# Kernel tuning notes

Measured on AMD Instinct MI355X. Metric: run time of the kernel, lower is better.

## Reference

```python
import jax, jax.numpy as jnp
import numpy as np

IN_DIMS = 1024
K = 8


def setup_inputs() -> dict:
    key = jax.random.key(0)
    ks = jax.random.split(key, 7)
    s = 1.0 / np.sqrt(IN_DIMS)
    x = jax.random.normal(ks[0], (8, 2048, IN_DIMS), dtype=jnp.float32)
    Wq = jax.random.uniform(ks[1], (IN_DIMS, K), jnp.float32, -s, s)
    bq = jax.random.uniform(ks[2], (K,), jnp.float32, -s, s)
    Wk = jax.random.uniform(ks[3], (IN_DIMS, K), jnp.float32, -s, s)
    bk = jax.random.uniform(ks[4], (K,), jnp.float32, -s, s)
    Wv = jax.random.uniform(ks[5], (IN_DIMS, IN_DIMS), jnp.float32, -s, s)
    bv = jax.random.uniform(ks[6], (IN_DIMS,), jnp.float32, -s, s)
    return {"x": x, "Wq": Wq, "bq": bq, "Wk": Wk, "bk": bk, "Wv": Wv, "bv": bv}


def reference(x, Wq, bq, Wk, bk, Wv, bv):
    # x: [B,S,D]; rank-k projections
    q = jnp.einsum('bsd,dk->bsk', x, Wq) + bq        # [B,S,k]
    k = jnp.einsum('bsd,dk->bsk', x, Wk) + bk        # [B,S,k]
    energy = jnp.einsum('bik,bjk->bij', q, k)        # [B,S,S] (unscaled)
    attention = jax.nn.softmax(energy, axis=-1)
    value = jnp.einsum('bsd,de->bse', x, Wv) + bv    # [B,S,D]
    out = jnp.einsum('bij,bjd->bid', attention, value)
    return (out, attention)
```

## Files before the change

kernel.cpp:

```cpp
#include <hip/hip_runtime.h>


typedef __attribute__((ext_vector_type(8))) __bf16 bf16x8;
typedef __attribute__((ext_vector_type(4))) __bf16 bf16x4;
typedef __attribute__((ext_vector_type(4))) float  f32x4;
typedef unsigned int u32;

#define GLB_CAST(p) ((const __attribute__((address_space(1))) u32*)(p))
#define LDS_CAST(p) ((__attribute__((address_space(3))) u32*)(p))

#define S_BARRIER() { __builtin_amdgcn_s_barrier(); __builtin_amdgcn_sched_barrier(0); }
#define LGKM0()     { asm volatile("s_waitcnt lgkmcnt(0)" ::: "memory"); __builtin_amdgcn_sched_barrier(0); }
#define VMCNT8()    { asm volatile("s_waitcnt vmcnt(8)" ::: "memory"); __builtin_amdgcn_sched_barrier(0); }
#define VMCNT0()    { asm volatile("s_waitcnt vmcnt(0)" ::: "memory"); __builtin_amdgcn_sched_barrier(0); }

static constexpr int    Bn   = 8;
static constexpr int    S    = 2048;
static constexpr int    Dd   = 1024;
static constexpr int    Mtot = Bn * S;
static constexpr size_t OUT0 = (size_t)Bn * S * Dd;

static constexpr size_t OFF_XBF  = 0;
static constexpr size_t OFF_WVT  = OFF_XBF  + (size_t)Mtot * Dd * 2;
static constexpr size_t OFF_WQKT = OFF_WVT  + (size_t)Dd * Dd * 2;
static constexpr size_t OFF_Q    = OFF_WQKT + (size_t)16 * Dd * 2;
static constexpr size_t OFF_K    = OFF_Q    + (size_t)Mtot * 8 * 4;
static constexpr size_t OFF_VT   = OFF_K    + (size_t)Mtot * 8 * 4;
static constexpr size_t OFF_ATTB = OFF_VT   + (size_t)Bn * Dd * S * 2;
static constexpr size_t WS_NEED  = OFF_ATTB + (size_t)Bn * S * S * 2;

__global__ __launch_bounds__(256) void prep_kernel(
    const float* __restrict__ x, const float* __restrict__ Wq,
    const float* __restrict__ Wk, const float* __restrict__ Wv,
    __bf16* __restrict__ xbf, __bf16* __restrict__ wvt, __bf16* __restrict__ wqkT)
{
    __shared__ float lt[64][65];
    int bid = blockIdx.x, t = threadIdx.x;
    if (bid < 4096) {
        #pragma unroll
        for (int i = 0; i < 4; ++i) {
            size_t idx4 = (size_t)i * 1048576 + (size_t)bid * 256 + t;
            f32x4 v = ((const f32x4*)x)[idx4];
            bf16x4 o;
            #pragma unroll
            for (int c = 0; c < 4; ++c) o[c] = (__bf16)v[c];
            ((bf16x4*)xbf)[idx4] = o;
        }
    } else if (bid < 4352) {
        int tile = bid - 4096;
        int tr = tile >> 4, tc = tile & 15;
        int r0 = t >> 6, c = t & 63;
        #pragma unroll
        for (int i = 0; i < 16; ++i) {
            int row = i * 4 + r0;
            lt[row][c] = Wv[(size_t)(tr * 64 + row) * 1024 + tc * 64 + c];
        }
        __syncthreads();
        #pragma unroll
        for (int i = 0; i < 16; ++i) {
            int er = i * 4 + r0;
            wvt[(size_t)(tc * 64 + er) * 1024 + tr * 64 + c] = (__bf16)lt[c][er];
        }
    } else {
        int lb = bid - 4352;
        #pragma unroll
        for (int i = 0; i < 4; ++i) {
            int idx = (lb * 4 + i) * 256 + t;
            int n = idx >> 10, d = idx & 1023;
            float v = (n < 8) ? Wq[d * 8 + n] : Wk[d * 8 + (n & 7)];
            wqkT[n * 1024 + d] = (__bf16)v;
        }
    }
}

__global__ __launch_bounds__(256) void qk_proj_kernel(
    const __bf16* __restrict__ xbf, const __bf16* __restrict__ wqkT,
    const float* __restrict__ bq, const float* __restrict__ bk,
    float* __restrict__ qb, float* __restrict__ kb)
{
    int t = threadIdx.x, l = t & 63, w = t >> 6;
    int mbase = (blockIdx.x * 4 + w) * 16;
    f32x4 acc = {0.f, 0.f, 0.f, 0.f};
    const __bf16* ar = xbf + (size_t)(mbase + (l & 15)) * 1024 + ((l >> 4) << 3);
    const __bf16* br = wqkT + (size_t)(l & 15) * 1024 + ((l >> 4) << 3);
    #pragma unroll 8
    for (int kk = 0; kk < 1024; kk += 32) {
        bf16x8 a = *(const bf16x8*)(ar + kk);
        bf16x8 b = *(const bf16x8*)(br + kk);
        acc = __builtin_amdgcn_mfma_f32_16x16x32_bf16(a, b, acc, 0, 0, 0);
    }
    int n = l & 15;
    float bias = (n < 8) ? bq[n] : bk[n & 7];
    #pragma unroll
    for (int r = 0; r < 4; ++r) {
        int m = mbase + ((l >> 4) << 2) + r;
        float v = acc[r] + bias;
        if (n < 8) qb[m * 8 + n] = v;
        else       kb[m * 8 + (n & 7)] = v;
    }
}

__global__ __launch_bounds__(256) void softmax_kernel(
    const float* __restrict__ qb, const float* __restrict__ kb,
    float* __restrict__ attnF, __bf16* __restrict__ attnB)
{
    int bid = blockIdx.x;
    int b = bid >> 6, chunk = bid & 63;
    int t = threadIdx.x, l = t & 63, w = t >> 6;
    float kr[8][8];
    const float* kbb = kb + ((size_t)b << 14);
    #pragma unroll
    for (int jj = 0; jj < 8; ++jj) {
        f32x4 v0 = *(const f32x4*)(kbb + (size_t)(t * 8 + jj) * 8);
        f32x4 v1 = *(const f32x4*)(kbb + (size_t)(t * 8 + jj) * 8 + 4);
        #pragma unroll
        for (int c = 0; c < 4; ++c) { kr[jj][c] = v0[c]; kr[jj][4 + c] = v1[c]; }
    }
    __shared__ float redm[4], reds[4];
    const float* qrow = qb + ((size_t)b << 14);
    for (int ii = 0; ii < 32; ++ii) {
        int i = (chunk << 5) + ii;
        f32x4 q0 = *(const f32x4*)(qrow + (size_t)i * 8);
        f32x4 q1 = *(const f32x4*)(qrow + (size_t)i * 8 + 4);
        float e[8];
        #pragma unroll
        for (int jj = 0; jj < 8; ++jj) {
            float s = q0[0] * kr[jj][0];
            s = fmaf(q0[1], kr[jj][1], s);
            s = fmaf(q0[2], kr[jj][2], s);
            s = fmaf(q0[3], kr[jj][3], s);
            s = fmaf(q1[0], kr[jj][4], s);
            s = fmaf(q1[1], kr[jj][5], s);
            s = fmaf(q1[2], kr[jj][6], s);
            s = fmaf(q1[3], kr[jj][7], s);
            e[jj] = s;
        }
        float mx = e[0];
        #pragma unroll
        for (int jj = 1; jj < 8; ++jj) mx = fmaxf(mx, e[jj]);
        #pragma unroll
        for (int d = 1; d < 64; d <<= 1) mx = fmaxf(mx, __shfl_xor(mx, d));
        if (l == 0) redm[w] = mx;
        __syncthreads();
        mx = fmaxf(fmaxf(redm[0], redm[1]), fmaxf(redm[2], redm[3]));
        float p[8], sum = 0.f;
        #pragma unroll
        for (int jj = 0; jj < 8; ++jj) { p[jj] = __expf(e[jj] - mx); sum += p[jj]; }
        #pragma unroll
        for (int d = 1; d < 64; d <<= 1) sum += __shfl_xor(sum, d);
        if (l == 0) reds[w] = sum;
        __syncthreads();
        float T = (reds[0] + reds[1]) + (reds[2] + reds[3]);
        float inv = 1.0f / T;
        size_t off = (((size_t)b << 11) + i) * 2048 + (size_t)t * 8;
        f32x4 o0, o1; bf16x8 ob;
        #pragma unroll
        for (int c = 0; c < 4; ++c) {
            o0[c] = p[c] * inv; o1[c] = p[4 + c] * inv;
            ob[c] = (__bf16)o0[c]; ob[4 + c] = (__bf16)o1[c];
        }
        *(f32x4*)(attnF + off) = o0;
        *(f32x4*)(attnF + off + 4) = o1;
        *(bf16x8*)(attnB + off) = ob;
    }
}

template<int LDA>
__device__ __forceinline__ void stageA(const __bf16* Ab, char* smem,
    int slot, int kk, int c, int rowin, int sl8, int wid)
{
    __builtin_amdgcn_global_load_lds(
        GLB_CAST(Ab + (size_t)(c * 64 + rowin) * LDA + kk + sl8 * 8),
        LDS_CAST(smem + slot * 65536 + c * 8192 + wid * 1024), 16, 0, 0);
}
template<int LDA>
__device__ __forceinline__ void stageB(const __bf16* Bb, char* smem,
    int slot, int kk, int c, int rowin, int sl8, int wid)
{
    __builtin_amdgcn_global_load_lds(
        GLB_CAST(Bb + (size_t)(c * 64 + rowin) * LDA + kk + sl8 * 8),
        LDS_CAST(smem + slot * 65536 + 32768 + c * 8192 + wid * 1024), 16, 0, 0);
}

template<int MODE>
__global__ __launch_bounds__(512, 2) void gemm_kernel(
    const __bf16* __restrict__ A, const __bf16* __restrict__ Bt,
    float* __restrict__ outF, __bf16* __restrict__ outVt,
    const float* __restrict__ bv)
{
    constexpr int LDA = (MODE == 0) ? 1024 : 2048;
    constexpr int NT  = LDA / 64;
    __shared__ __align__(1024) char smem[131072];

    int bid = blockIdx.x;
    int wg = ((bid & 7) << 5) | (bid >> 3);
    int t = threadIdx.x, l = t & 63;
    int wid = t >> 6;
    int wmr = wid >> 2, wnc = wid & 3;

    int mblk, nblk, bb = 0;
    size_t aoff, boff;
    if constexpr (MODE == 0) {
        mblk = wg >> 2; nblk = wg & 3;
        aoff = (size_t)mblk * 256 * LDA; boff = 0;
    } else {
        bb = wg >> 5; int r = wg & 31;
        mblk = r >> 2; nblk = r & 3;
        aoff = (size_t)bb * S * S + (size_t)mblk * 256 * LDA;
        boff = (size_t)bb * Dd * S;
    }
    const __bf16* Ab = A + aoff;
    const __bf16* Bb = Bt + boff + (size_t)nblk * 256 * LDA;

    int rowin = t >> 3;
    int sl8 = (t & 7) ^ (rowin & 7);
    int lr = l & 15, lk = l >> 4;

    f32x4 acc[8][4] = {};

    #pragma unroll
    for (int c = 0; c < 4; ++c) {
        stageA<LDA>(Ab, smem, 0, 0, c, rowin, sl8, wid);
        stageB<LDA>(Bb, smem, 0, 0, c, rowin, sl8, wid);
    }
    #pragma unroll
    for (int c = 0; c < 4; ++c) {
        stageA<LDA>(Ab, smem, 1, 64, c, rowin, sl8, wid);
        stageB<LDA>(Bb, smem, 1, 64, c, rowin, sl8, wid);
    }
    VMCNT8();
    S_BARRIER();

    for (int tt = 0; tt < NT; ++tt) {
        int s = tt & 1;
        const __bf16* Asl = (const __bf16*)(smem + s * 65536);
        const __bf16* Bsl = (const __bf16*)(smem + s * 65536 + 32768);
        bool pf = (tt + 2 < NT);
        int kk2 = (tt + 2) * 64;

        bf16x8 aLo[2][4], aHi[2][4], bLo[2][2], bHi[2][2];

        #pragma unroll
        for (int ks = 0; ks < 2; ++ks) {
            int sa = ks * 4 + lk;
            #pragma unroll
            for (int i = 0; i < 4; ++i) {
                int ra = wmr * 128 + i * 16 + lr;
                aLo[ks][i] = *(const bf16x8*)&Asl[ra * 64 + ((sa ^ (ra & 7)) << 3)];
            }
            #pragma unroll
            for (int j = 0; j < 2; ++j) {
                int rb = wnc * 64 + j * 16 + lr;
                bLo[ks][j] = *(const bf16x8*)&Bsl[rb * 64 + ((sa ^ (rb & 7)) << 3)];
            }
        }
        S_BARRIER(); LGKM0();
        __builtin_amdgcn_s_setprio(1);
        #pragma unroll
        for (int ks = 0; ks < 2; ++ks)
            #pragma unroll
            for (int i = 0; i < 4; ++i)
                #pragma unroll
                for (int j = 0; j < 2; ++j)
                    acc[i][j] = __builtin_amdgcn_mfma_f32_16x16x32_bf16(aLo[ks][i], bLo[ks][j], acc[i][j], 0, 0, 0);
        __builtin_amdgcn_s_setprio(0);
        S_BARRIER();

        #pragma unroll
        for (int ks = 0; ks < 2; ++ks) {
            int sa = ks * 4 + lk;
            #pragma unroll
            for (int j = 0; j < 2; ++j) {
                int rb = wnc * 64 + (j + 2) * 16 + lr;
                bHi[ks][j] = *(const bf16x8*)&Bsl[rb * 64 + ((sa ^ (rb & 7)) << 3)];
            }
        }
        if (pf) {
            stageA<LDA>(Ab, smem, s, kk2, 0, rowin, sl8, wid);
            stageA<LDA>(Ab, smem, s, kk2, 2, rowin, sl8, wid);
        }
        S_BARRIER(); LGKM0();
        __builtin_amdgcn_s_setprio(1);
        #pragma unroll
        for (int ks = 0; ks < 2; ++ks)
            #pragma unroll
            for (int i = 0; i < 4; ++i)
                #pragma unroll
                for (int j = 0; j < 2; ++j)
                    acc[i][2 + j] = __builtin_amdgcn_mfma_f32_16x16x32_bf16(aLo[ks][i], bHi[ks][j], acc[i][2 + j], 0, 0, 0);
        __builtin_amdgcn_s_setprio(0);
        S_BARRIER();

        #pragma unroll
        for (int ks = 0; ks < 2; ++ks) {
            int sa = ks * 4 + lk;
            #pragma unroll
            for (int i = 0; i < 4; ++i) {
                int ra = wmr * 128 + (i + 4) * 16 + lr;
                aHi[ks][i] = *(const bf16x8*)&Asl[ra * 64 + ((sa ^ (ra & 7)) << 3)];
            }
        }
        if (pf) {
            #pragma unroll
            for (int c = 0; c < 4; ++c)
                stageB<LDA>(Bb, smem, s, kk2, c, rowin, sl8, wid);
        }
        S_BARRIER(); LGKM0();
        __builtin_amdgcn_s_setprio(1);
        #pragma unroll
        for (int ks = 0; ks < 2; ++ks)
            #pragma unroll
            for (int i = 0; i < 4; ++i)
                #pragma unroll
                for (int j = 0; j < 2; ++j)
                    acc[4 + i][2 + j] = __builtin_amdgcn_mfma_f32_16x16x32_bf16(aHi[ks][i], bHi[ks][j], acc[4 + i][2 + j], 0, 0, 0);
        __builtin_amdgcn_s_setprio(0);
        S_BARRIER();

        if (pf) {
            stageA<LDA>(Ab, smem, s, kk2, 1, rowin, sl8, wid);
            stageA<LDA>(Ab, smem, s, kk2, 3, rowin, sl8, wid);
        }
        S_BARRIER();
        __builtin_amdgcn_s_setprio(1);
        #pragma unroll
        for (int ks = 0; ks < 2; ++ks)
            #pragma unroll
            for (int i = 0; i < 4; ++i)
                #pragma unroll
                for (int j = 0; j < 2; ++j)
                    acc[4 + i][j] = __builtin_amdgcn_mfma_f32_16x16x32_bf16(aHi[ks][i], bLo[ks][j], acc[4 + i][j], 0, 0, 0);
        __builtin_amdgcn_s_setprio(0);

        if (tt == NT - 1) break;
        S_BARRIER();
        if (pf) { VMCNT8(); } else { VMCNT0(); }
        S_BARRIER();
    }

    if constexpr (MODE == 0) {
        #pragma unroll
        for (int j = 0; j < 4; ++j) {
            int e = (nblk << 8) + wnc * 64 + j * 16 + lr;
            float bias = bv[e];
            #pragma unroll
            for (int i = 0; i < 8; ++i) {
                int m0 = (mblk << 8) + wmr * 128 + i * 16 + (lk << 2);
                int b = m0 >> 11, s0 = m0 & 2047;
                bf16x4 o;
                #pragma unroll
                for (int r = 0; r < 4; ++r) o[r] = (__bf16)(acc[i][j][r] + bias);
                *(bf16x4*)&outVt[(((size_t)(b << 10) + e) << 11) + s0] = o;
            }
        }
    } else {
        float* ob = outF + (size_t)bb * S * Dd;
        #pragma unroll
        for (int i = 0; i < 8; ++i) {
            int m0 = (mblk << 8) + wmr * 128 + i * 16 + (lk << 2);
            #pragma unroll
            for (int j = 0; j < 4; ++j) {
                int e = (nblk << 8) + wnc * 64 + j * 16 + lr;
                #pragma unroll
                for (int r = 0; r < 4; ++r)
                    ob[(size_t)(m0 + r) * 1024 + e] = acc[i][j][r];
            }
        }
    }
}

extern "C" void kernel_launch(void* const* d_in, const int* in_sizes, int n_in,
                              void* d_out, int out_size, void* d_ws, size_t ws_size,
                              hipStream_t stream)
{
    const float* x  = (const float*)d_in[0];
    const float* Wq = (const float*)d_in[1];
    const float* bq = (const float*)d_in[2];
    const float* Wk = (const float*)d_in[3];
    const float* bk = (const float*)d_in[4];
    const float* Wv = (const float*)d_in[5];
    const float* bv = (const float*)d_in[6];

    float* outp  = (float*)d_out;
    float* attnF = outp + OUT0;

    if (ws_size < WS_NEED) return;
    char* ws = (char*)d_ws;
    __bf16* xbf   = (__bf16*)(ws + OFF_XBF);
    __bf16* wvt   = (__bf16*)(ws + OFF_WVT);
    __bf16* wqkT  = (__bf16*)(ws + OFF_WQKT);
    float*  qbuf  = (float*)(ws + OFF_Q);
    float*  kbuf  = (float*)(ws + OFF_K);
    __bf16* vt    = (__bf16*)(ws + OFF_VT);
    __bf16* attnB = (__bf16*)(ws + OFF_ATTB);

    prep_kernel<<<4368, 256, 0, stream>>>(x, Wq, Wk, Wv, xbf, wvt, wqkT);
    qk_proj_kernel<<<256, 256, 0, stream>>>(xbf, wqkT, bq, bk, qbuf, kbuf);
    gemm_kernel<0><<<256, 512, 0, stream>>>(xbf, wvt, nullptr, vt, bv);
    softmax_kernel<<<512, 256, 0, stream>>>(qbuf, kbuf, attnF, attnB);
    gemm_kernel<1><<<256, 512, 0, stream>>>(attnB, vt, outp, nullptr, nullptr);
}
```

Baseline: 196.3 us.

## Fuse value-projection GEMM and softmax into one interleaved heterogeneous launch

Merges the x·Wv GEMM and the softmax kernel into a single launch whose blocks are interleaved by segment: some blocks run a new, smaller 128x128-tile single-buffered GEMM and others run the softmax. The aim is to overlap the compute-bound GEMM with the store-bound softmax (which writes the large fp32 and bf16 attention matrices) and to remove one kernel boundary. In exchange, the value GEMM loses the highly tuned 256x256 double-buffered pipeline. It now uses a simpler kernel with a sync per K-step, which may make the GEMM itself slower.

Measured after the change: 187.1 us. 4.7% less time.

```diff
diff --git a/kernel.cpp b/kernel.cpp
--- a/kernel.cpp
+++ b/kernel.cpp
@@ -21,12 +21,12 @@
 static constexpr size_t OUT0 = (size_t)Bn * S * Dd;
 
 static constexpr size_t OFF_XBF  = 0;
-static constexpr size_t OFF_WVT  = OFF_XBF  + (size_t)Mtot * Dd * 2;
-static constexpr size_t OFF_WQKT = OFF_WVT  + (size_t)Dd * Dd * 2;
+static constexpr size_t OFF_WVT  = OFF_XBF + (size_t)Mtot * Dd * 2;
+static constexpr size_t OFF_WQKT = OFF_WVT + (size_t)Dd * Dd * 2;
 static constexpr size_t OFF_Q    = OFF_WQKT + (size_t)16 * Dd * 2;
-static constexpr size_t OFF_K    = OFF_Q    + (size_t)Mtot * 8 * 4;
-static constexpr size_t OFF_VT   = OFF_K    + (size_t)Mtot * 8 * 4;
-static constexpr size_t OFF_ATTB = OFF_VT   + (size_t)Bn * Dd * S * 2;
+static constexpr size_t OFF_K    = OFF_Q   + (size_t)Mtot * 8 * 4;
+static constexpr size_t OFF_VT   = OFF_K   + (size_t)Mtot * 8 * 4;
+static constexpr size_t OFF_ATTB = OFF_VT  + (size_t)Bn * Dd * S * 2;
 static constexpr size_t WS_NEED  = OFF_ATTB + (size_t)Bn * S * S * 2;
 
 __global__ __launch_bounds__(256) void prep_kernel(
@@ -100,96 +100,176 @@
     }
 }
 
-__global__ __launch_bounds__(256) void softmax_kernel(
+__global__ __launch_bounds__(256) void fused_gs_kernel(
+    const __bf16* __restrict__ xbf, const __bf16* __restrict__ wvt,
+    const float* __restrict__ bv,
     const float* __restrict__ qb, const float* __restrict__ kb,
-    float* __restrict__ attnF, __bf16* __restrict__ attnB)
-{
-    int bid = blockIdx.x;
-    int b = bid >> 6, chunk = bid & 63;
-    int t = threadIdx.x, l = t & 63, w = t >> 6;
-    float kr[8][8];
-    const float* kbb = kb + ((size_t)b << 14);
-    #pragma unroll
-    for (int jj = 0; jj < 8; ++jj) {
-        f32x4 v0 = *(const f32x4*)(kbb + (size_t)(t * 8 + jj) * 8);
-        f32x4 v1 = *(const f32x4*)(kbb + (size_t)(t * 8 + jj) * 8 + 4);
-        #pragma unroll
-        for (int c = 0; c < 4; ++c) { kr[jj][c] = v0[c]; kr[jj][4 + c] = v1[c]; }
-    }
+    __bf16* __restrict__ vtOut, float* __restrict__ attnF,
+    __bf16* __restrict__ attnB)
+{
+    __shared__ __align__(1024) char smem[32768];
     __shared__ float redm[4], reds[4];
-    const float* qrow = qb + ((size_t)b << 14);
-    for (int ii = 0; ii < 32; ++ii) {
-        int i = (chunk << 5) + ii;
-        f32x4 q0 = *(const f32x4*)(qrow + (size_t)i * 8);
-        f32x4 q1 = *(const f32x4*)(qrow + (size_t)i * 8 + 4);
-        float e[8];
+    int bid = blockIdx.x, t = threadIdx.x;
+    int seg = bid >> 8;
+    int gid = -1, sid = -1;
+    if (seg == 0) gid = bid;
+    else if (seg == 1) sid = bid - 256;
+    else if (seg == 2) gid = bid - 256;
+    else if (seg == 3) sid = bid - 512;
+    else gid = bid - 512;
+
+    if (sid < 0) {
+        int g = ((gid & 7) << 7) | (gid >> 3);
+        int mblk = g >> 3, nblk = g & 7;
+        int l = t & 63, wid = t >> 6;
+        int wmr = wid >> 1, wnc = wid & 1;
+        int lr = l & 15, lk = l >> 4;
+
+        int srow = t >> 3;
+        int ssl  = (t & 7) ^ (srow & 7);
+        const __bf16* gA = xbf + (size_t)(mblk * 128 + srow) * 1024 + ssl * 8;
+        const __bf16* gB = wvt + (size_t)(nblk * 128 + srow) * 1024 + ssl * 8;
+
+        int s0 = (lk ^ (lr & 7)) << 3;
+        int s1 = ((lk ^ 4) ^ (lr & 7)) << 3;
+        int offA0 = (wmr * 64 + lr) * 64 + s0;
+        int offA1 = (wmr * 64 + lr) * 64 + s1;
+        int offB0 = (wnc * 64 + lr) * 64 + s0;
+        int offB1 = (wnc * 64 + lr) * 64 + s1;
+
+        f32x4 acc[4][4] = {};
+
+        for (int tt = 0; tt < 16; ++tt) {
+            int kk = tt * 64;
+            #pragma unroll
+            for (int c = 0; c < 4; ++c) {
+                __builtin_amdgcn_global_load_lds(
+                    GLB_CAST(gA + (size_t)c * 32 * 1024 + kk),
+                    LDS_CAST(smem + c * 4096 + wid * 1024), 16, 0, 0);
+                __builtin_amdgcn_global_load_lds(
+                    GLB_CAST(gB + (size_t)c * 32 * 1024 + kk),
+                    LDS_CAST(smem + 16384 + c * 4096 + wid * 1024), 16, 0, 0);
+            }
+            __syncthreads();
+            const __bf16* As = (const __bf16*)smem;
+            const __bf16* Bs = (const __bf16*)(smem + 16384);
+            bf16x8 af[4], bfr[4];
+            #pragma unroll
+            for (int i = 0; i < 4; ++i) af[i]  = *(const bf16x8*)(As + offA0 + i * 1024);
+            #pragma unroll
+            for (int j = 0; j < 4; ++j) bfr[j] = *(const bf16x8*)(Bs + offB0 + j * 1024);
+            #pragma unroll
+            for (int i = 0; i < 4; ++i)
+                #pragma unroll
+                for (int j = 0; j < 4; ++j)
+                    acc[i][j] = __builtin_amdgcn_mfma_f32_16x16x32_bf16(af[i], bfr[j], acc[i][j], 0, 0, 0);
+            #pragma unroll
+            for (int i = 0; i < 4; ++i) af[i]  = *(const bf16x8*)(As + offA1 + i * 1024);
+            #pragma unroll
+            for (int j = 0; j < 4; ++j) bfr[j] = *(const bf16x8*)(Bs + offB1 + j * 1024);
+            #pragma unroll
+            for (int i = 0; i < 4; ++i)
+                #pragma unroll
+                for (int j = 0; j < 4; ++j)
+                    acc[i][j] = __builtin_amdgcn_mfma_f32_16x16x32_bf16(af[i], bfr[j], acc[i][j], 0, 0, 0);
+            __syncthreads();
+        }
+
+        #pragma unroll
+        for (int j = 0; j < 4; ++j) {
+            int e = (nblk << 7) + wnc * 64 + j * 16 + lr;
+            float bias = bv[e];
+            #pragma unroll
+            for (int i = 0; i < 4; ++i) {
+                int m0 = (mblk << 7) + wmr * 64 + i * 16 + (lk << 2);
+                int b = m0 >> 11, sA = m0 & 2047;
+                bf16x4 o;
+                #pragma unroll
+                for (int r = 0; r < 4; ++r) o[r] = (__bf16)(acc[i][j][r] + bias);
+                *(bf16x4*)&vtOut[(((size_t)(b << 10) + e) << 11) + sA] = o;
+            }
+        }
+    } else {
+        int b = sid >> 6, chunk = sid & 63;
+        int l = t & 63, w = t >> 6;
+        float kr[8][8];
+        const float* kbb = kb + ((size_t)b << 14);
         #pragma unroll
         for (int jj = 0; jj < 8; ++jj) {
-            float s = q0[0] * kr[jj][0];
-            s = fmaf(q0[1], kr[jj][1], s);
-            s = fmaf(q0[2], kr[jj][2], s);
-            s = fmaf(q0[3], kr[jj][3], s);
-            s = fmaf(q1[0], kr[jj][4], s);
-            s = fmaf(q1[1], kr[jj][5], s);
-            s = fmaf(q1[2], kr[jj][6], s);
-            s = fmaf(q1[3], kr[jj][7], s);
-            e[jj] = s;
-        }
-        float mx = e[0];
-        #pragma unroll
-        for (int jj = 1; jj < 8; ++jj) mx = fmaxf(mx, e[jj]);
-        #pragma unroll
-        for (int d = 1; d < 64; d <<= 1) mx = fmaxf(mx, __shfl_xor(mx, d));
-        if (l == 0) redm[w] = mx;
-        __syncthreads();
-        mx = fmaxf(fmaxf(redm[0], redm[1]), fmaxf(redm[2], redm[3]));
-        float p[8], sum = 0.f;
-        #pragma unroll
-        for (int jj = 0; jj < 8; ++jj) { p[jj] = __expf(e[jj] - mx); sum += p[jj]; }
-        #pragma unroll
-        for (int d = 1; d < 64; d <<= 1) sum += __shfl_xor(sum, d);
-        if (l == 0) reds[w] = sum;
-        __syncthreads();
-        float T = (reds[0] + reds[1]) + (reds[2] + reds[3]);
-        float inv = 1.0f / T;
-        size_t off = (((size_t)b << 11) + i) * 2048 + (size_t)t * 8;
-        f32x4 o0, o1; bf16x8 ob;
-        #pragma unroll
-        for (int c = 0; c < 4; ++c) {
-            o0[c] = p[c] * inv; o1[c] = p[4 + c] * inv;
-            ob[c] = (__bf16)o0[c]; ob[4 + c] = (__bf16)o1[c];
-        }
-        *(f32x4*)(attnF + off) = o0;
-        *(f32x4*)(attnF + off + 4) = o1;
-        *(bf16x8*)(attnB + off) = ob;
-    }
-}
-
-template<int LDA>
-__device__ __forceinline__ void stageA(const __bf16* Ab, char* smem,
+            f32x4 v0 = *(const f32x4*)(kbb + (size_t)(t * 8 + jj) * 8);
+            f32x4 v1 = *(const f32x4*)(kbb + (size_t)(t * 8 + jj) * 8 + 4);
+            #pragma unroll
+            for (int c = 0; c < 4; ++c) { kr[jj][c] = v0[c]; kr[jj][4 + c] = v1[c]; }
+        }
+        const float* qrow = qb + ((size_t)b << 14);
+        for (int ii = 0; ii < 32; ++ii) {
+            int i = (chunk << 5) + ii;
+            f32x4 q0 = *(const f32x4*)(qrow + (size_t)i * 8);
+            f32x4 q1 = *(const f32x4*)(qrow + (size_t)i * 8 + 4);
+            float e[8];
+            #pragma unroll
+            for (int jj = 0; jj < 8; ++jj) {
+                float s = q0[0] * kr[jj][0];
+                s = fmaf(q0[1], kr[jj][1], s);
+                s = fmaf(q0[2], kr[jj][2], s);
+                s = fmaf(q0[3], kr[jj][3], s);
+                s = fmaf(q1[0], kr[jj][4], s);
+                s = fmaf(q1[1], kr[jj][5], s);
+                s = fmaf(q1[2], kr[jj][6], s);
+                s = fmaf(q1[3], kr[jj][7], s);
+                e[jj] = s;
+            }
+            float mx = e[0];
+            #pragma unroll
+            for (int jj = 1; jj < 8; ++jj) mx = fmaxf(mx, e[jj]);
+            #pragma unroll
+            for (int d = 1; d < 64; d <<= 1) mx = fmaxf(mx, __shfl_xor(mx, d));
+            if (l == 0) redm[w] = mx;
+            __syncthreads();
+            mx = fmaxf(fmaxf(redm[0], redm[1]), fmaxf(redm[2], redm[3]));
+            float p[8], sum = 0.f;
+            #pragma unroll
+            for (int jj = 0; jj < 8; ++jj) { p[jj] = __expf(e[jj] - mx); sum += p[jj]; }
+            #pragma unroll
+            for (int d = 1; d < 64; d <<= 1) sum += __shfl_xor(sum, d);
+            if (l == 0) reds[w] = sum;
+            __syncthreads();
+            float T = (reds[0] + reds[1]) + (reds[2] + reds[3]);
+            float inv = 1.0f / T;
+            size_t off = (((size_t)b << 11) + i) * 2048 + (size_t)t * 8;
+            f32x4 o0, o1; bf16x8 ob;
+            #pragma unroll
+            for (int c = 0; c < 4; ++c) {
+                o0[c] = p[c] * inv; o1[c] = p[4 + c] * inv;
+                ob[c] = (__bf16)o0[c]; ob[4 + c] = (__bf16)o1[c];
+            }
+            *(f32x4*)(attnF + off) = o0;
+            *(f32x4*)(attnF + off + 4) = o1;
+            *(bf16x8*)(attnB + off) = ob;
+        }
+    }
+}
+
+__device__ __forceinline__ void g1_stageA(const __bf16* Ab, char* smem,
     int slot, int kk, int c, int rowin, int sl8, int wid)
 {
     __builtin_amdgcn_global_load_lds(
-        GLB_CAST(Ab + (size_t)(c * 64 + rowin) * LDA + kk + sl8 * 8),
+        GLB_CAST(Ab + (size_t)(c * 64 + rowin) * 2048 + kk + sl8 * 8),
         LDS_CAST(smem + slot * 65536 + c * 8192 + wid * 1024), 16, 0, 0);
 }
-template<int LDA>
-__device__ __forceinline__ void stageB(const __bf16* Bb, char* smem,
+__device__ __forceinline__ void g1_stageB(const __bf16* Bb, char* smem,
     int slot, int kk, int c, int rowin, int sl8, int wid)
 {
     __builtin_amdgcn_global_load_lds(
-        GLB_CAST(Bb + (size_t)(c * 64 + rowin) * LDA + kk + sl8 * 8),
+        GLB_CAST(Bb + (size_t)(c * 64 + rowin) * 2048 + kk + sl8 * 8),
         LDS_CAST(smem + slot * 65536 + 32768 + c * 8192 + wid * 1024), 16, 0, 0);
 }
 
-template<int MODE>
-__global__ __launch_bounds__(512, 2) void gemm_kernel(
+__global__ __launch_bounds__(512, 2) void gemm1_kernel(
     const __bf16* __restrict__ A, const __bf16* __restrict__ Bt,
-    float* __restrict__ outF, __bf16* __restrict__ outVt,
-    const float* __restrict__ bv)
-{
-    constexpr int LDA = (MODE == 0) ? 1024 : 2048;
-    constexpr int NT  = LDA / 64;
+    float* __restrict__ outF)
+{
+    constexpr int NT = 32;
     __shared__ __align__(1024) char smem[131072];
 
     int bid = blockIdx.x;
@@ -198,19 +278,10 @@
     int wid = t >> 6;
     int wmr = wid >> 2, wnc = wid & 3;
 
-    int mblk, nblk, bb = 0;
-    size_t aoff, boff;
-    if constexpr (MODE == 0) {
-        mblk = wg >> 2; nblk = wg & 3;
-        aoff = (size_t)mblk * 256 * LDA; boff = 0;
-    } else {
-        bb = wg >> 5; int r = wg & 31;
-        mblk = r >> 2; nblk = r & 3;
-        aoff = (size_t)bb * S * S + (size_t)mblk * 256 * LDA;
-        boff = (size_t)bb * Dd * S;
-    }
-    const __bf16* Ab = A + aoff;
-    const __bf16* Bb = Bt + boff + (size_t)nblk * 256 * LDA;
+    int bb = wg >> 5; int r = wg & 31;
+    int mblk = r >> 2, nblk = r & 3;
+    const __bf16* Ab = A + (size_t)bb * S * S + (size_t)mblk * 256 * 2048;
+    const __bf16* Bb = Bt + (size_t)bb * Dd * S + (size_t)nblk * 256 * 2048;
 
     int rowin = t >> 3;
     int sl8 = (t & 7) ^ (rowin & 7);
@@ -220,13 +291,13 @@
 
     #pragma unroll
     for (int c = 0; c < 4; ++c) {
-        stageA<LDA>(Ab, smem, 0, 0, c, rowin, sl8, wid);
-        stageB<LDA>(Bb, smem, 0, 0, c, rowin, sl8, wid);
+        g1_stageA(Ab, smem, 0, 0, c, rowin, sl8, wid);
+        g1_stageB(Bb, smem, 0, 0, c, rowin, sl8, wid);
     }
     #pragma unroll
     for (int c = 0; c < 4; ++c) {
-        stageA<LDA>(Ab, smem, 1, 64, c, rowin, sl8, wid);
-        stageB<LDA>(Bb, smem, 1, 64, c, rowin, sl8, wid);
+        g1_stageA(Ab, smem, 1, 64, c, rowin, sl8, wid);
+        g1_stageB(Bb, smem, 1, 64, c, rowin, sl8, wid);
     }
     VMCNT8();
     S_BARRIER();
@@ -276,8 +347,8 @@
             }
         }
         if (pf) {
-            stageA<LDA>(Ab, smem, s, kk2, 0, rowin, sl8, wid);
-            stageA<LDA>(Ab, smem, s, kk2, 2, rowin, sl8, wid);
+            g1_stageA(Ab, smem, s, kk2, 0, rowin, sl8, wid);
+            g1_stageA(Ab, smem, s, kk2, 2, rowin, sl8, wid);
         }
         S_BARRIER(); LGKM0();
         __builtin_amdgcn_s_setprio(1);
@@ -303,7 +374,7 @@
         if (pf) {
             #pragma unroll
             for (int c = 0; c < 4; ++c)
-                stageB<LDA>(Bb, smem, s, kk2, c, rowin, sl8, wid);
+                g1_stageB(Bb, smem, s, kk2, c, rowin, sl8, wid);
         }
         S_BARRIER(); LGKM0();
         __builtin_amdgcn_s_setprio(1);
@@ -318,8 +389,8 @@
         S_BARRIER();
 
         if (pf) {
-            stageA<LDA>(Ab, smem, s, kk2, 1, rowin, sl8, wid);
-            stageA<LDA>(Ab, smem, s, kk2, 3, rowin, sl8, wid);
+            g1_stageA(Ab, smem, s, kk2, 1, rowin, sl8, wid);
+            g1_stageA(Ab, smem, s, kk2, 3, rowin, sl8, wid);
         }
         S_BARRIER();
         __builtin_amdgcn_s_setprio(1);
@@ -338,33 +409,16 @@
         S_BARRIER();
     }
 
-    if constexpr (MODE == 0) {
+    float* ob = outF + (size_t)bb * S * Dd;
+    #pragma unroll
+    for (int i = 0; i < 8; ++i) {
+        int m0 = (mblk << 8) + wmr * 128 + i * 16 + (lk << 2);
         #pragma unroll
         for (int j = 0; j < 4; ++j) {
             int e = (nblk << 8) + wnc * 64 + j * 16 + lr;
-            float bias = bv[e];
-            #pragma unroll
-            for (int i = 0; i < 8; ++i) {
-                int m0 = (mblk << 8) + wmr * 128 + i * 16 + (lk << 2);
-                int b = m0 >> 11, s0 = m0 & 2047;
-                bf16x4 o;
-                #pragma unroll
-                for (int r = 0; r < 4; ++r) o[r] = (__bf16)(acc[i][j][r] + bias);
-                *(bf16x4*)&outVt[(((size_t)(b << 10) + e) << 11) + s0] = o;
-            }
-        }
-    } else {
-        float* ob = outF + (size_t)bb * S * Dd;
-        #pragma unroll
-        for (int i = 0; i < 8; ++i) {
-            int m0 = (mblk << 8) + wmr * 128 + i * 16 + (lk << 2);
-            #pragma unroll
-            for (int j = 0; j < 4; ++j) {
-                int e = (nblk << 8) + wnc * 64 + j * 16 + lr;
-                #pragma unroll
-                for (int r = 0; r < 4; ++r)
-                    ob[(size_t)(m0 + r) * 1024 + e] = acc[i][j][r];
-            }
+            #pragma unroll
+            for (int r = 0; r < 4; ++r)
+                ob[(size_t)(m0 + r) * 1024 + e] = acc[i][j][r];
         }
     }
 }
@@ -396,7 +450,6 @@
 
     prep_kernel<<<4368, 256, 0, stream>>>(x, Wq, Wk, Wv, xbf, wvt, wqkT);
     qk_proj_kernel<<<256, 256, 0, stream>>>(xbf, wqkT, bq, bk, qbuf, kbuf);
-    gemm_kernel<0><<<256, 512, 0, stream>>>(xbf, wvt, nullptr, vt, bv);
-    softmax_kernel<<<512, 256, 0, stream>>>(qbuf, kbuf, attnF, attnB);
-    gemm_kernel<1><<<256, 512, 0, stream>>>(attnB, vt, outp, nullptr, nullptr);
-}
+    fused_gs_kernel<<<1536, 256, 0, stream>>>(xbf, wvt, bv, qbuf, kbuf, vt, attnF, attnB);
+    gemm1_kernel<<<256, 512, 0, stream>>>(attnB, vt, outp);
+}
```
